# Kernel tuning notes

Hardware: AMD Instinct MI355X
Metric: run time of the kernel (lower is better)

Reference implementation:

```python
import jax, jax.numpy as jnp
import numpy as np
from jax import lax

B, C, H, W = 8, 1, 256, 256
BIG = float(H + W)  # larger than any possible in-image distance


def _dist_1d_along_h(feat):
    # feat: bool (B,H,W). Exact 1D distance along axis 1 to nearest True pixel.
    def step(d, f):
        d = jnp.where(f, 0.0, d + 1.0)
        return d, d

    init = jnp.full((feat.shape[0], feat.shape[2]), BIG, dtype=jnp.float32)
    ft = jnp.moveaxis(feat, 1, 0)  # (H,B,W)
    _, fwd = lax.scan(step, init, ft)
    _, bwd = lax.scan(step, init, ft[::-1])
    g = jnp.minimum(fwd, bwd[::-1])  # (H,B,W)
    return jnp.moveaxis(g, 0, 1)  # (B,H,W)


def _edt(feat):
    # Exact 2D Euclidean distance transform to nearest True pixel.
    # Decomposition: D2(i,j) = min_{j'} ( g(i,j')^2 + (j-j')^2 ),
    # where g is the exact 1D vertical distance within each column.
    g = jnp.minimum(_dist_1d_along_h(feat), BIG)
    g2 = g * g  # (B,H,W')
    j = jnp.arange(feat.shape[2], dtype=jnp.float32)
    offs = (j[:, None] - j[None, :]) ** 2  # (W, W')
    d2 = jnp.min(g2[:, :, None, :] + offs[None, None, :, :], axis=-1)  # (B,H,W)
    return jnp.sqrt(d2)


def _level_set(targets):
    # Faithful port of compute_level_set_function.
    m = targets[:, 0] != 0  # (B,H,W) foreground
    # scipy.distance_transform_edt(mask): distance of nonzero pixels to nearest zero -> features = background
    dist_inside = _edt(~m)
    # distance_transform_edt(1-mask): features = foreground
    dist_outside = _edt(m)
    phi = dist_outside - dist_inside
    denom = jnp.max(jnp.abs(phi), axis=(1, 2), keepdims=True) + 1e-8
    phi = phi / denom
    has_fg = jnp.any(m, axis=(1, 2), keepdims=True)
    phi = jnp.where(has_fg, phi, 0.0)  # empty-mask short-circuit -> zeros
    return phi[:, None].astype(jnp.float32)  # (B,1,H,W)


def setup_inputs() -> dict:
    key = jax.random.key(0)
    k1, k2 = jax.random.split(key)
    predictions = jax.random.normal(k1, (B, C, H, W), dtype=jnp.float32)
    targets = jax.random.randint(k2, (B, C, H, W), 0, 2, dtype=jnp.int32)
    return {"predictions": predictions, "targets": targets}


def reference(predictions, targets):
    probs = jax.nn.sigmoid(predictions)
    phi_G = _level_set(targets)
    return jnp.mean(phi_G * probs)
```

## Files before the change

### kernel.cpp

```cpp
#include <hip/hip_runtime.h>
#include <math.h>

#define BB 8
#define HH 256
#define WW 256
#define NPIX (BB*HH*WW)
#define NROWS (BB*HH)


__global__ void maskbuild(const int* __restrict__ tgt,
                          unsigned* __restrict__ fg_words) {
    int blk = blockIdx.x;
    int b = blk >> 3, band = blk & 7;
    int j = threadIdx.x;
    const int* base = tgt + b * (HH * WW) + (band * 32) * WW + j;
    unsigned bits = 0;
    #pragma unroll
    for (int r = 0; r < 32; ++r)
        bits |= (base[r * WW] != 0 ? 1u : 0u) << r;
    fg_words[b * 2048 + band * 256 + j] = bits;
}

__global__ void edt_row(const unsigned* __restrict__ fg_words,
                        const float* __restrict__ pred,
                        float* __restrict__ part_max,
                        double* __restrict__ part_sum,
                        int* __restrict__ part_fg) {
    __shared__ unsigned maskL[256 * 9];
    __shared__ float sB[3 * WW];
    __shared__ float sF[3 * WW];
    __shared__ float wmax[4];
    __shared__ double wsum[4];
    __shared__ int wfg[4];

    int row = blockIdx.x;
    int b = row >> 8, i = row & 255;
    int j = threadIdx.x;

    float x = pred[row * WW + j];

    const unsigned* mb = fg_words + b * 2048;
    #pragma unroll
    for (int w = 0; w < 8; ++w)
        maskL[j * 9 + w] = mb[w * 256 + j];
    __syncthreads();

    const int BIGI = 1 << 20;
    int pF = -BIGI, pB = -BIGI, nF = BIGI, nB = BIGI;
    #pragma unroll
    for (int w = 0; w < 4; ++w) {
        unsigned long long v = (unsigned long long)maskL[j * 9 + 2 * w]
                             | ((unsigned long long)maskL[j * 9 + 2 * w + 1] << 32);
        unsigned long long g = ~v;
        int d = i - 64 * w;
        unsigned long long bf = (d >= 63) ? v : ((d < 0) ? 0ull : (v & (~0ull >> (63 - d))));
        unsigned long long bb = (d >= 63) ? g : ((d < 0) ? 0ull : (g & (~0ull >> (63 - d))));
        if (bf) pF = 64 * w + 63 - __builtin_clzll(bf);
        if (bb) pB = 64 * w + 63 - __builtin_clzll(bb);
        unsigned long long af = (d <= 0) ? v : ((d > 63) ? 0ull : (v & (~0ull << d)));
        unsigned long long ab = (d <= 0) ? g : ((d > 63) ? 0ull : (g & (~0ull << d)));
        if (af) nF = min(nF, 64 * w + __builtin_ctzll(af));
        if (ab) nB = min(nB, 64 * w + __builtin_ctzll(ab));
    }
    int gF = min(min(i - pF, nF - i), 512);
    int gB = min(min(i - pB, nB - i), 512);
    bool isFg = (gF == 0);
    unsigned long long fgb = __ballot(isFg);

    float fF = (float)gF, fB = (float)gB;
    sF[j] = 1e30f; sF[2 * WW + j] = 1e30f; sF[WW + j] = fF * fF;
    sB[j] = 1e30f; sB[2 * WW + j] = 1e30f; sB[WW + j] = fB * fB;
    __syncthreads();

    const float* sp = isFg ? sB : sF;
    float m = isFg ? fB * fB : fF * fF;
    int idx = WW + j;
    for (int k = 1; k < WW; ++k) {
        float k2 = (float)(k * k);
        if (k2 >= m) break;
        m = fminf(m, sp[idx - k] + k2);
        m = fminf(m, sp[idx + k] + k2);
    }
    float dist = sqrtf(m);
    float phi = isFg ? -dist : dist;
    float prob = 1.0f / (1.0f + expf(-x));
    double sd = (double)(phi * prob);
    float mx = dist;

    #pragma unroll
    for (int off = 32; off; off >>= 1) {
        mx = fmaxf(mx, __shfl_down(mx, off));
        sd += __shfl_down(sd, off);
    }
    int wid = j >> 6;
    if ((j & 63) == 0) { wmax[wid] = mx; wsum[wid] = sd; wfg[wid] = (fgb != 0ull); }
    __syncthreads();
    if (j == 0) {
        part_max[row] = fmaxf(fmaxf(wmax[0], wmax[1]), fmaxf(wmax[2], wmax[3]));
        part_sum[row] = wsum[0] + wsum[1] + wsum[2] + wsum[3];
        part_fg[row] = wfg[0] | wfg[1] | wfg[2] | wfg[3];
    }
}

__global__ void reduce_out(const float* __restrict__ part_max,
                           const double* __restrict__ part_sum,
                           const int* __restrict__ part_fg,
                           float* __restrict__ out) {
    __shared__ double terms[8];
    int tx = threadIdx.x;
    int wv = tx >> 6, l = tx & 63;
    #pragma unroll
    for (int q = 0; q < 2; ++q) {
        int b = wv * 2 + q;
        int base = b * HH;
        float mx = fmaxf(fmaxf(part_max[base + l], part_max[base + l + 64]),
                         fmaxf(part_max[base + l + 128], part_max[base + l + 192]));
        double sd = part_sum[base + l] + part_sum[base + l + 64]
                  + part_sum[base + l + 128] + part_sum[base + l + 192];
        int fg = part_fg[base + l] | part_fg[base + l + 64]
               | part_fg[base + l + 128] | part_fg[base + l + 192];
        #pragma unroll
        for (int off = 32; off; off >>= 1) {
            mx = fmaxf(mx, __shfl_down(mx, off));
            sd += __shfl_down(sd, off);
            fg |= __shfl_down(fg, off);
        }
        if (l == 0) terms[b] = fg ? sd / ((double)mx + 1e-8) : 0.0;
    }
    __syncthreads();
    if (tx == 0) {
        double t = 0.0;
        #pragma unroll
        for (int b = 0; b < BB; ++b) t += terms[b];
        out[0] = (float)(t / (double)NPIX);
    }
}

extern "C" void kernel_launch(void* const* d_in, const int* in_sizes, int n_in,
                              void* d_out, int out_size, void* d_ws, size_t ws_size,
                              hipStream_t stream) {
    const float* pred = (const float*)d_in[0];
    const int* tgt = (const int*)d_in[1];
    float* out = (float*)d_out;

    char* ws = (char*)d_ws;
    float* part_max = (float*)ws;
    double* part_sum = (double*)(ws + 8192);
    int* part_fg = (int*)(ws + 24576);
    unsigned* fg_words = (unsigned*)(ws + 32768);

    maskbuild<<<64, 256, 0, stream>>>(tgt, fg_words);
    edt_row<<<NROWS, WW, 0, stream>>>(fg_words, pred, part_max, part_sum, part_fg);
    reduce_out<<<1, 256, 0, stream>>>(part_max, part_sum, part_fg, out);
}
```

Measured before the change: 64.38 us.

## Fuse final reduction into EDT kernel via last-block atomic counters

```diff
diff --git a/kernel.cpp b/kernel.cpp
--- a/kernel.cpp
+++ b/kernel.cpp
@@ -9,7 +9,9 @@
 
 
 __global__ void maskbuild(const int* __restrict__ tgt,
-                          unsigned* __restrict__ fg_words) {
+                          unsigned* __restrict__ fg_words,
+                          unsigned* __restrict__ cnt) {
+    if (blockIdx.x == 0 && threadIdx.x < 9) cnt[threadIdx.x] = 0u;
     int blk = blockIdx.x;
     int b = blk >> 3, band = blk & 7;
     int j = threadIdx.x;
@@ -25,13 +27,16 @@
                         const float* __restrict__ pred,
                         float* __restrict__ part_max,
                         double* __restrict__ part_sum,
-                        int* __restrict__ part_fg) {
-    __shared__ unsigned maskL[256 * 9];
+                        int* __restrict__ part_fg,
+                        unsigned* __restrict__ cnt,
+                        double* __restrict__ terms,
+                        float* __restrict__ out) {
     __shared__ float sB[3 * WW];
     __shared__ float sF[3 * WW];
     __shared__ float wmax[4];
     __shared__ double wsum[4];
     __shared__ int wfg[4];
+    __shared__ int amLast, amLastG;
 
     int row = blockIdx.x;
     int b = row >> 8, i = row & 255;
@@ -40,17 +45,16 @@
     float x = pred[row * WW + j];
 
     const unsigned* mb = fg_words + b * 2048;
+    unsigned mw[8];
     #pragma unroll
-    for (int w = 0; w < 8; ++w)
-        maskL[j * 9 + w] = mb[w * 256 + j];
-    __syncthreads();
+    for (int w = 0; w < 8; ++w) mw[w] = mb[w * 256 + j];
 
     const int BIGI = 1 << 20;
     int pF = -BIGI, pB = -BIGI, nF = BIGI, nB = BIGI;
     #pragma unroll
     for (int w = 0; w < 4; ++w) {
-        unsigned long long v = (unsigned long long)maskL[j * 9 + 2 * w]
-                             | ((unsigned long long)maskL[j * 9 + 2 * w + 1] << 32);
+        unsigned long long v = (unsigned long long)mw[2 * w]
+                             | ((unsigned long long)mw[2 * w + 1] << 32);
         unsigned long long g = ~v;
         int d = i - 64 * w;
         unsigned long long bf = (d >= 63) ? v : ((d < 0) ? 0ull : (v & (~0ull >> (63 - d))));
@@ -99,40 +103,42 @@
         part_max[row] = fmaxf(fmaxf(wmax[0], wmax[1]), fmaxf(wmax[2], wmax[3]));
         part_sum[row] = wsum[0] + wsum[1] + wsum[2] + wsum[3];
         part_fg[row] = wfg[0] | wfg[1] | wfg[2] | wfg[3];
-    }
-}
-
-__global__ void reduce_out(const float* __restrict__ part_max,
-                           const double* __restrict__ part_sum,
-                           const int* __restrict__ part_fg,
-                           float* __restrict__ out) {
-    __shared__ double terms[8];
-    int tx = threadIdx.x;
-    int wv = tx >> 6, l = tx & 63;
-    #pragma unroll
-    for (int q = 0; q < 2; ++q) {
-        int b = wv * 2 + q;
-        int base = b * HH;
-        float mx = fmaxf(fmaxf(part_max[base + l], part_max[base + l + 64]),
-                         fmaxf(part_max[base + l + 128], part_max[base + l + 192]));
-        double sd = part_sum[base + l] + part_sum[base + l + 64]
-                  + part_sum[base + l + 128] + part_sum[base + l + 192];
-        int fg = part_fg[base + l] | part_fg[base + l + 64]
-               | part_fg[base + l + 128] | part_fg[base + l + 192];
-        #pragma unroll
-        for (int off = 32; off; off >>= 1) {
-            mx = fmaxf(mx, __shfl_down(mx, off));
-            sd += __shfl_down(sd, off);
-            fg |= __shfl_down(fg, off);
-        }
-        if (l == 0) terms[b] = fg ? sd / ((double)mx + 1e-8) : 0.0;
+        __threadfence();
+        unsigned old = atomicAdd(&cnt[b], 1u);
+        amLast = (old == (unsigned)(HH - 1));
     }
     __syncthreads();
-    if (tx == 0) {
-        double t = 0.0;
+    if (!amLast) return;
+
+    __threadfence();
+    int base = b * HH;
+    float mx2 = part_max[base + j];
+    double sd2 = part_sum[base + j];
+    int fg2 = part_fg[base + j];
+    #pragma unroll
+    for (int off = 32; off; off >>= 1) {
+        mx2 = fmaxf(mx2, __shfl_down(mx2, off));
+        sd2 += __shfl_down(sd2, off);
+        fg2 |= __shfl_down(fg2, off);
+    }
+    if ((j & 63) == 0) { wmax[wid] = mx2; wsum[wid] = sd2; wfg[wid] = fg2; }
+    __syncthreads();
+    if (j == 0) {
+        float M = fmaxf(fmaxf(wmax[0], wmax[1]), fmaxf(wmax[2], wmax[3]));
+        double S = wsum[0] + wsum[1] + wsum[2] + wsum[3];
+        int F = wfg[0] | wfg[1] | wfg[2] | wfg[3];
+        terms[b] = F ? S / ((double)M + 1e-8) : 0.0;
+        __threadfence();
+        unsigned o2 = atomicAdd(&cnt[8], 1u);
+        amLastG = (o2 == (unsigned)(BB - 1));
+    }
+    __syncthreads();
+    if (amLastG && j == 0) {
+        __threadfence();
+        double tot = 0.0;
         #pragma unroll
-        for (int b = 0; b < BB; ++b) t += terms[b];
-        out[0] = (float)(t / (double)NPIX);
+        for (int q = 0; q < BB; ++q) tot += terms[q];
+        out[0] = (float)(tot / (double)NPIX);
     }
 }
 
@@ -148,8 +154,10 @@
     double* part_sum = (double*)(ws + 8192);
     int* part_fg = (int*)(ws + 24576);
     unsigned* fg_words = (unsigned*)(ws + 32768);
+    unsigned* cnt = (unsigned*)(ws + 98304);
+    double* terms = (double*)(ws + 98368);
 
-    maskbuild<<<64, 256, 0, stream>>>(tgt, fg_words);
-    edt_row<<<NROWS, WW, 0, stream>>>(fg_words, pred, part_max, part_sum, part_fg);
-    reduce_out<<<1, 256, 0, stream>>>(part_max, part_sum, part_fg, out);
+    maskbuild<<<64, 256, 0, stream>>>(tgt, fg_words, cnt);
+    edt_row<<<NROWS, WW, 0, stream>>>(fg_words, pred, part_max, part_sum,
+                                      part_fg, cnt, terms, out);
 }
```

New measurement: 113.3 us. 76.0% more time.
